# Optimization experiments

Measured on AMD Instinct MI355X. Metric: run time of the kernel, lower is better.

The kernel has to match this reference:

```python
import jax, jax.numpy as jnp
import numpy as np

B, C_IN, C_OUT, T, R, CO = 8, 64, 64, 32, 32, 32


def setup_inputs() -> dict:
    key = jax.random.key(0)
    ks = jax.random.split(key, 8)
    scale = 1.0 / np.sqrt(C_IN)  # nn.Linear default uniform(-1/sqrt(in), 1/sqrt(in))
    w = lambda k: jax.random.uniform(k, (C_OUT, C_IN), jnp.float32, -scale, scale)
    return {
        "x": jax.random.normal(ks[0], (B, C_IN, T, R, CO), jnp.float32),
        "w_self": w(ks[1]),
        "w_tp": w(ks[2]),
        "w_tm": w(ks[3]),
        "w_rp": w(ks[4]),
        "w_rm": w(ks[5]),
        "w_cp": w(ks[6]),
        "w_cm": w(ks[7]),
    }


def _proj(v, w):
    # v: [B, t, r, c, C_in], w: [C_out, C_in] (nn.Linear layout)
    return jnp.einsum('btrci,oi->btrco', v, w)


def _shift_pad(a, axis, front):
    # pad 1 slice at front (True) or back (False) along `axis` of a 5-D tensor
    pads = [(0, 0)] * 5
    pads[axis] = (1, 0) if front else (0, 1)
    return jnp.pad(a, pads)


def reference(x, w_self, w_tp, w_tm, w_rp, w_rm, w_cp, w_cm):
    xp = jnp.transpose(x, (0, 2, 3, 4, 1))  # [B, T, R, Co, C_in]
    out = _proj(xp, w_self)
    if xp.shape[1] > 1:
        out = out + _shift_pad(_proj(xp[:, :-1], w_tp), 1, True)
        out = out + _shift_pad(_proj(xp[:, 1:], w_tm), 1, False)
    if xp.shape[2] > 1:
        out = out + _shift_pad(_proj(xp[:, :, :-1], w_rp), 2, True)
        out = out + _shift_pad(_proj(xp[:, :, 1:], w_rm), 2, False)
    if xp.shape[3] > 1:
        out = out + _shift_pad(_proj(xp[:, :, :, :-1], w_cp), 3, True)
        out = out + _shift_pad(_proj(xp[:, :, :, 1:], w_cm), 3, False)
    return jnp.transpose(out, (0, 4, 1, 2, 3))  # [B, C_out, T, R, Co]
```

## Files before the change

kernel.cpp:

```cpp
#include <hip/hip_runtime.h>


#define SB 32768
#define CIN 64
#define COUT 64
#define NB 8

typedef short s16x8 __attribute__((ext_vector_type(8)));
typedef __bf16 bf16x8 __attribute__((ext_vector_type(8)));
typedef float f32x4 __attribute__((ext_vector_type(4)));

__device__ __forceinline__ unsigned f2bf(float f) {
    unsigned u = __float_as_uint(f);
    u += 0x7FFFu + ((u >> 16) & 1u);
    return u >> 16;
}
__device__ __forceinline__ unsigned pk2(float lo, float hi) {
    return f2bf(lo) | (f2bf(hi) << 16);
}

__global__ __launch_bounds__(256) void wprep_kernel(const float* __restrict__ w0,
                            const float* __restrict__ w1, const float* __restrict__ w2,
                            const float* __restrict__ w3, const float* __restrict__ w4,
                            const float* __restrict__ w5, const float* __restrict__ w6,
                            unsigned short* __restrict__ ws) {
    int tap = blockIdx.x;
    int tid = threadIdx.x;
    const float* w = (tap == 0) ? w0 : (tap == 1) ? w1 : (tap == 2) ? w2
                   : (tap == 3) ? w3 : (tap == 4) ? w4 : (tap == 5) ? w5 : w6;
    unsigned p[8];
#pragma unroll
    for (int j = 0; j < 8; ++j)
        p[j] = pk2(w[tid * 16 + 2 * j], w[tid * 16 + 2 * j + 1]);
    uint4* dp = (uint4*)(ws + tap * 4096 + tid * 16);
    dp[0] = make_uint4(p[0], p[1], p[2], p[3]);
    dp[1] = make_uint4(p[4], p[5], p[6], p[7]);
}

__global__ __launch_bounds__(256) void prep_kernel(const float* __restrict__ x,
                            const float* __restrict__ w0, const float* __restrict__ w1,
                            const float* __restrict__ w2, const float* __restrict__ w3,
                            const float* __restrict__ w4, const float* __restrict__ w5,
                            const float* __restrict__ w6,
                            unsigned short* __restrict__ ws) {
    int bid = blockIdx.x;
    int tid = threadIdx.x;
    if (bid >= 1024) {
        int tap = bid - 1024;
        const float* w = (tap == 0) ? w0 : (tap == 1) ? w1 : (tap == 2) ? w2
                       : (tap == 3) ? w3 : (tap == 4) ? w4 : (tap == 5) ? w5 : w6;
        unsigned p[8];
#pragma unroll
        for (int j = 0; j < 8; ++j)
            p[j] = pk2(w[tid * 16 + 2 * j], w[tid * 16 + 2 * j + 1]);
        uint4* dp = (uint4*)(ws + tap * 4096 + tid * 16);
        dp[0] = make_uint4(p[0], p[1], p[2], p[3]);
        dp[1] = make_uint4(p[4], p[5], p[6], p[7]);
        return;
    }
    __shared__ uint4 l[2048];
    int lbid = ((bid & 7) << 7) | (bid >> 3);
    int b = lbid >> 7;
    int sblk = (lbid & 127) << 8;
    unsigned short* xq = ws + 7 * 4096;
    const float* xp = x + (size_t)b * CIN * SB + sblk + tid;
#pragma unroll
    for (int c = 0; c < 4; ++c) {
        unsigned pk[8];
#pragma unroll
        for (int u = 0; u < 8; ++u)
            pk[u] = pk2(xp[(size_t)(c * 16 + 2 * u) * SB],
                        xp[(size_t)(c * 16 + 2 * u + 1) * SB]);
        l[tid * 8 + ((2 * c) ^ (tid & 7))] = make_uint4(pk[0], pk[1], pk[2], pk[3]);
        l[tid * 8 + ((2 * c + 1) ^ (tid & 7))] = make_uint4(pk[4], pk[5], pk[6], pk[7]);
    }
    __syncthreads();
    uint4* dst = (uint4*)(xq + ((size_t)b * SB + sblk) * 64);
#pragma unroll
    for (int k = 0; k < 8; ++k) {
        int idx = k * 256 + tid;
        int row = idx >> 3;
        int col = idx & 7;
        dst[idx] = l[row * 8 + (col ^ (row & 7))];
    }
}

__global__ __launch_bounds__(256) void conv2_kernel(const unsigned short* __restrict__ xq,
                                                    const unsigned short* __restrict__ wq,
                                                    float* __restrict__ out) {
    int bid = blockIdx.x;
    int lbid = ((bid & 7) << 7) | (bid >> 3);
    int b = lbid >> 7;
    int sblk = (lbid & 127) << 8;
    int tid = threadIdx.x;
    int lane = tid & 63;
    int wv = tid >> 6;
    int lo = lane & 15;
    int quad = lane >> 4;
    int sbase = sblk + wv * 64;
    int t = sblk >> 10;
    const unsigned short* xb = xq + (size_t)b * (CIN * SB);

    f32x4 acc[4][4];
#pragma unroll
    for (int mt = 0; mt < 4; ++mt)
#pragma unroll
        for (int nt = 0; nt < 4; ++nt)
            acc[mt][nt] = (f32x4){0.f, 0.f, 0.f, 0.f};

    int s_m[4], r_m[4], c_m[4];
#pragma unroll
    for (int mt = 0; mt < 4; ++mt) {
        int s = sbase + mt * 16 + lo;
        s_m[mt] = s;
        r_m[mt] = (s >> 5) & 31;
        c_m[mt] = s & 31;
    }

    auto load_b = [&](const unsigned short* wt, int ks, int nt) -> bf16x8 {
        const unsigned short* bp = wt + (nt * 16 + lo) * 64 + ks * 32 + quad * 8;
        return __builtin_bit_cast(bf16x8, *(const s16x8*)bp);
    };

    auto run_tap = [&](int tap, int d, const bool ok[4]) {
        const unsigned short* wt = wq + tap * 4096;
#pragma unroll
        for (int ks = 0; ks < 2; ++ks) {
            bf16x8 bf[4];
#pragma unroll
            for (int nt = 0; nt < 4; ++nt) bf[nt] = load_b(wt, ks, nt);
#pragma unroll
            for (int mt = 0; mt < 4; ++mt) {
                int s = s_m[mt] + d;
                s = s < 0 ? 0 : s;
                s = s > SB - 1 ? SB - 1 : s;
                s16x8 raw = *(const s16x8*)(xb + (size_t)s * 64 + ks * 32 + quad * 8);
                s16x8 zz = {0, 0, 0, 0, 0, 0, 0, 0};
                raw = ok[mt] ? raw : zz;
                bf16x8 af = __builtin_bit_cast(bf16x8, raw);
#pragma unroll
                for (int nt = 0; nt < 4; ++nt)
                    acc[mt][nt] = __builtin_amdgcn_mfma_f32_16x16x32_bf16(af, bf[nt], acc[mt][nt], 0, 0, 0);
            }
        }
    };

    {
        bool ok_all[4] = {true, true, true, true};
        run_tap(0, 0, ok_all);
        if (t > 0)  run_tap(1, -1024, ok_all);
        if (t < 31) run_tap(2, 1024, ok_all);
    }
    {
        bool ok[4];
#pragma unroll
        for (int mt = 0; mt < 4; ++mt) ok[mt] = (r_m[mt] > 0);
        run_tap(3, -32, ok);
#pragma unroll
        for (int mt = 0; mt < 4; ++mt) ok[mt] = (r_m[mt] < 31);
        run_tap(4, 32, ok);
#pragma unroll
        for (int mt = 0; mt < 4; ++mt) ok[mt] = (c_m[mt] > 0);
        run_tap(5, -1, ok);
#pragma unroll
        for (int mt = 0; mt < 4; ++mt) ok[mt] = (c_m[mt] < 31);
        run_tap(6, 1, ok);
    }

#pragma unroll
    for (int mt = 0; mt < 4; ++mt) {
#pragma unroll
        for (int nt = 0; nt < 4; ++nt) {
            int o = nt * 16 + lo;
            size_t off = ((size_t)(b * COUT + o)) * SB + sbase + mt * 16 + quad * 4;
            *(f32x4*)(out + off) = acc[mt][nt];
        }
    }
}

__global__ __launch_bounds__(256) void conv_kernel(const float* __restrict__ x,
                                                   const unsigned short* __restrict__ wq,
                                                   float* __restrict__ out) {
    __shared__ uint4 alds[2560];
    int bid = blockIdx.x;
    int b = bid >> 7;
    int sblk = (bid & 127) << 8;
    int tid = threadIdx.x;
    const float* xb = x + (size_t)b * CIN * SB;

    {
        int rl = 32 + tid;
        const float* xp = xb + sblk + tid;
#pragma unroll
        for (int c = 0; c < 4; ++c) {
            unsigned pk[8];
#pragma unroll
            for (int u = 0; u < 8; ++u)
                pk[u] = pk2(xp[(size_t)(c * 16 + 2 * u) * SB],
                            xp[(size_t)(c * 16 + 2 * u + 1) * SB]);
            alds[rl * 8 + ((2 * c) ^ (rl & 7))] = make_uint4(pk[0], pk[1], pk[2], pk[3]);
            alds[rl * 8 + ((2 * c + 1) ^ (rl & 7))] = make_uint4(pk[4], pk[5], pk[6], pk[7]);
        }
    }
    {
        int hrow = tid & 63;
        int rl = (hrow < 32) ? hrow : hrow + 256;
        int s = sblk - 32 + rl;
        s = max(0, min(SB - 1, s));
        int ic = tid >> 6;
        const float* xp = xb + s + (size_t)(ic * 16) * SB;
        unsigned pk[8];
#pragma unroll
        for (int u = 0; u < 8; ++u)
            pk[u] = pk2(xp[(size_t)(2 * u) * SB], xp[(size_t)(2 * u + 1) * SB]);
        alds[rl * 8 + ((2 * ic) ^ (rl & 7))] = make_uint4(pk[0], pk[1], pk[2], pk[3]);
        alds[rl * 8 + ((2 * ic + 1) ^ (rl & 7))] = make_uint4(pk[4], pk[5], pk[6], pk[7]);
    }
    __syncthreads();

    int lane = tid & 63;
    int wv = tid >> 6;
    int lo = lane & 15;
    int quad = lane >> 4;
    int sbase = sblk + wv * 64;
    int t = sblk >> 10;

    f32x4 acc[4][4];
#pragma unroll
    for (int mt = 0; mt < 4; ++mt)
#pragma unroll
        for (int nt = 0; nt < 4; ++nt)
            acc[mt][nt] = (f32x4){0.f, 0.f, 0.f, 0.f};

    int r_m[4], c_m[4], rl[4];
#pragma unroll
    for (int mt = 0; mt < 4; ++mt) {
        int s = sbase + mt * 16 + lo;
        r_m[mt] = (s >> 5) & 31;
        c_m[mt] = s & 31;
        rl[mt] = s - sblk + 32;
    }

    auto load_b = [&](const unsigned short* wt, int ks, int nt) -> bf16x8 {
        const unsigned short* bp = wt + (nt * 16 + lo) * 64 + ks * 32 + quad * 8;
        return __builtin_bit_cast(bf16x8, *(const s16x8*)bp);
    };

    auto run_tap_lds = [&](int tap, int d, const bool ok[4]) {
        const unsigned short* wt = wq + tap * 4096;
#pragma unroll
        for (int ks = 0; ks < 2; ++ks) {
            bf16x8 bf[4];
#pragma unroll
            for (int nt = 0; nt < 4; ++nt) bf[nt] = load_b(wt, ks, nt);
            int j = ks * 4 + quad;
#pragma unroll
            for (int mt = 0; mt < 4; ++mt) {
                int row = rl[mt] + d;
                s16x8 raw = *((const s16x8*)alds + row * 8 + (j ^ (row & 7)));
                s16x8 zz = {0, 0, 0, 0, 0, 0, 0, 0};
                raw = ok[mt] ? raw : zz;
                bf16x8 af = __builtin_bit_cast(bf16x8, raw);
#pragma unroll
                for (int nt = 0; nt < 4; ++nt)
                    acc[mt][nt] = __builtin_amdgcn_mfma_f32_16x16x32_bf16(af, bf[nt], acc[mt][nt], 0, 0, 0);
            }
        }
    };

    auto run_tap_gather = [&](int tap, int d) {
        const unsigned short* wt = wq + tap * 4096;
#pragma unroll
        for (int ks = 0; ks < 2; ++ks) {
            bf16x8 bf[4];
#pragma unroll
            for (int nt = 0; nt < 4; ++nt) bf[nt] = load_b(wt, ks, nt);
            const float* gp = xb + (size_t)(ks * 32 + quad * 8) * SB + d;
#pragma unroll
            for (int mt = 0; mt < 4; ++mt) {
                const float* ap = gp + sbase + mt * 16 + lo;
                unsigned pk[4];
#pragma unroll
                for (int u = 0; u < 4; ++u)
                    pk[u] = pk2(ap[(size_t)(2 * u) * SB], ap[(size_t)(2 * u + 1) * SB]);
                uint4 v = make_uint4(pk[0], pk[1], pk[2], pk[3]);
                bf16x8 af = __builtin_bit_cast(bf16x8, v);
#pragma unroll
                for (int nt = 0; nt < 4; ++nt)
                    acc[mt][nt] = __builtin_amdgcn_mfma_f32_16x16x32_bf16(af, bf[nt], acc[mt][nt], 0, 0, 0);
            }
        }
    };

    {
        bool ok_all[4] = {true, true, true, true};
        run_tap_lds(0, 0, ok_all);
    }
    if (t > 0)  run_tap_gather(1, -1024);
    if (t < 31) run_tap_gather(2, 1024);
    {
        bool ok[4];
#pragma unroll
        for (int mt = 0; mt < 4; ++mt) ok[mt] = (r_m[mt] > 0);
        run_tap_lds(3, -32, ok);
#pragma unroll
        for (int mt = 0; mt < 4; ++mt) ok[mt] = (r_m[mt] < 31);
        run_tap_lds(4, 32, ok);
#pragma unroll
        for (int mt = 0; mt < 4; ++mt) ok[mt] = (c_m[mt] > 0);
        run_tap_lds(5, -1, ok);
#pragma unroll
        for (int mt = 0; mt < 4; ++mt) ok[mt] = (c_m[mt] < 31);
        run_tap_lds(6, 1, ok);
    }

#pragma unroll
    for (int mt = 0; mt < 4; ++mt) {
#pragma unroll
        for (int nt = 0; nt < 4; ++nt) {
            int o = nt * 16 + lo;
            size_t off = ((size_t)(b * COUT + o)) * SB + sbase + mt * 16 + quad * 4;
            *(f32x4*)(out + off) = acc[mt][nt];
        }
    }
}

__global__ void fallback_kernel(const float* __restrict__ x,
                                const float* __restrict__ w0, const float* __restrict__ w1,
                                const float* __restrict__ w2, const float* __restrict__ w3,
                                const float* __restrict__ w4, const float* __restrict__ w5,
                                const float* __restrict__ w6,
                                float* __restrict__ out) {
    int bid = blockIdx.x;
    int b = bid >> 11;
    int og = (bid >> 7) & 15;
    int sblk = (bid & 127) << 8;
    int tid = threadIdx.x;
    __shared__ float wl[7][4][64];
    const float* wp[7] = {w0, w1, w2, w3, w4, w5, w6};
    for (int k = tid; k < 7 * 4 * 64; k += 256) {
        int tap = k >> 8, oo = (k >> 6) & 3, i = k & 63;
        wl[tap][oo][i] = wp[tap][(og * 4 + oo) * 64 + i];
    }
    __syncthreads();
    int s = sblk + tid;
    int t = s >> 10, r = (s >> 5) & 31, c = s & 31;
    const float* xb = x + (size_t)b * CIN * SB + s;
    float a0 = 0, a1 = 0, a2 = 0, a3 = 0;
    for (int i = 0; i < 64; ++i) {
        const float* xi = xb + (size_t)i * SB;
        float vs = xi[0];
        float vtp = (t > 0) ? xi[-1024] : 0.f;
        float vtm = (t < 31) ? xi[1024] : 0.f;
        float vrp = (r > 0) ? xi[-32] : 0.f;
        float vrm = (r < 31) ? xi[32] : 0.f;
        float vcp = (c > 0) ? xi[-1] : 0.f;
        float vcm = (c < 31) ? xi[1] : 0.f;
        a0 += wl[0][0][i] * vs + wl[1][0][i] * vtp + wl[2][0][i] * vtm + wl[3][0][i] * vrp + wl[4][0][i] * vrm + wl[5][0][i] * vcp + wl[6][0][i] * vcm;
        a1 += wl[0][1][i] * vs + wl[1][1][i] * vtp + wl[2][1][i] * vtm + wl[3][1][i] * vrp + wl[4][1][i] * vrm + wl[5][1][i] * vcp + wl[6][1][i] * vcm;
        a2 += wl[0][2][i] * vs + wl[1][2][i] * vtp + wl[2][2][i] * vtm + wl[3][2][i] * vrp + wl[4][2][i] * vrm + wl[5][2][i] * vcp + wl[6][2][i] * vcm;
        a3 += wl[0][3][i] * vs + wl[1][3][i] * vtp + wl[2][3][i] * vtm + wl[3][3][i] * vrp + wl[4][3][i] * vrm + wl[5][3][i] * vcp + wl[6][3][i] * vcm;
    }
    size_t obase = ((size_t)b * COUT + og * 4) * SB + s;
    out[obase] = a0;
    out[obase + SB] = a1;
    out[obase + 2 * (size_t)SB] = a2;
    out[obase + 3 * (size_t)SB] = a3;
}

extern "C" void kernel_launch(void* const* d_in, const int* in_sizes, int n_in,
                              void* d_out, int out_size, void* d_ws, size_t ws_size,
                              hipStream_t stream) {
    const float* x = (const float*)d_in[0];
    const float* w0 = (const float*)d_in[1];
    const float* w1 = (const float*)d_in[2];
    const float* w2 = (const float*)d_in[3];
    const float* w3 = (const float*)d_in[4];
    const float* w4 = (const float*)d_in[5];
    const float* w5 = (const float*)d_in[6];
    const float* w6 = (const float*)d_in[7];
    float* out = (float*)d_out;

    size_t need_w = (size_t)7 * 4096 * 2;
    size_t need_full = need_w + (size_t)NB * CIN * SB * 2;
    if (d_ws != nullptr && ws_size >= need_full) {
        unsigned short* wsp = (unsigned short*)d_ws;
        prep_kernel<<<1031, 256, 0, stream>>>(x, w0, w1, w2, w3, w4, w5, w6, wsp);
        conv2_kernel<<<1024, 256, 0, stream>>>(wsp + 7 * 4096, wsp, out);
    } else if (d_ws != nullptr && ws_size >= need_w) {
        unsigned short* wsp = (unsigned short*)d_ws;
        wprep_kernel<<<7, 256, 0, stream>>>(w0, w1, w2, w3, w4, w5, w6, wsp);
        conv_kernel<<<1024, 256, 0, stream>>>(x, wsp, out);
    } else {
        fallback_kernel<<<8 * 16 * 128, 256, 0, stream>>>(x, w0, w1, w2, w3, w4, w5, w6, out);
    }
}
```

Before: 178.9 us.

## Stage bf16 activation tile in LDS and split output channels across waves

The bf16 transpose prep kernel drops its LDS staging and uses more blocks, each thread reading float2 pairs and writing packed channel groups directly. The conv kernel now uses 512 threads: it loads a haloed 320-row activation tile into swizzled LDS for the self, r and c taps, and gathers only the t taps from global memory. Each wave computes half of the output channels and keeps all seven taps' weight fragments in registers. The aim is to cut redundant global reads of neighbour rows and per-tap weight reloads, at the cost of more registers and a block-wide barrier.

```diff
diff --git a/kernel.cpp b/kernel.cpp
--- a/kernel.cpp
+++ b/kernel.cpp
@@ -37,7 +37,7 @@
     dp[1] = make_uint4(p[4], p[5], p[6], p[7]);
 }
 
-__global__ __launch_bounds__(256) void prep_kernel(const float* __restrict__ x,
+__global__ __launch_bounds__(256) void prep2_kernel(const float* __restrict__ x,
                             const float* __restrict__ w0, const float* __restrict__ w1,
                             const float* __restrict__ w2, const float* __restrict__ w3,
                             const float* __restrict__ w4, const float* __restrict__ w5,
@@ -45,8 +45,8 @@
                             unsigned short* __restrict__ ws) {
     int bid = blockIdx.x;
     int tid = threadIdx.x;
-    if (bid >= 1024) {
-        int tap = bid - 1024;
+    if (bid >= 4096) {
+        int tap = bid - 4096;
         const float* w = (tap == 0) ? w0 : (tap == 1) ? w1 : (tap == 2) ? w2
                        : (tap == 3) ? w3 : (tap == 4) ? w4 : (tap == 5) ? w5 : w6;
         unsigned p[8];
@@ -58,36 +58,31 @@
         dp[1] = make_uint4(p[4], p[5], p[6], p[7]);
         return;
     }
-    __shared__ uint4 l[2048];
-    int lbid = ((bid & 7) << 7) | (bid >> 3);
-    int b = lbid >> 7;
-    int sblk = (lbid & 127) << 8;
+    int lbid = ((bid & 7) << 9) | (bid >> 3);
+    int b = lbid >> 9;
+    int i = (lbid & 511) * 256 + tid;
+    int cg = i & 7;
+    int s = (i >> 3) * 2;
+    const float* xb = x + (size_t)b * CIN * SB;
     unsigned short* xq = ws + 7 * 4096;
-    const float* xp = x + (size_t)b * CIN * SB + sblk + tid;
-#pragma unroll
-    for (int c = 0; c < 4; ++c) {
-        unsigned pk[8];
-#pragma unroll
-        for (int u = 0; u < 8; ++u)
-            pk[u] = pk2(xp[(size_t)(c * 16 + 2 * u) * SB],
-                        xp[(size_t)(c * 16 + 2 * u + 1) * SB]);
-        l[tid * 8 + ((2 * c) ^ (tid & 7))] = make_uint4(pk[0], pk[1], pk[2], pk[3]);
-        l[tid * 8 + ((2 * c + 1) ^ (tid & 7))] = make_uint4(pk[4], pk[5], pk[6], pk[7]);
-    }
-    __syncthreads();
-    uint4* dst = (uint4*)(xq + ((size_t)b * SB + sblk) * 64);
-#pragma unroll
-    for (int k = 0; k < 8; ++k) {
-        int idx = k * 256 + tid;
-        int row = idx >> 3;
-        int col = idx & 7;
-        dst[idx] = l[row * 8 + (col ^ (row & 7))];
-    }
-}
-
-__global__ __launch_bounds__(256) void conv2_kernel(const unsigned short* __restrict__ xq,
-                                                    const unsigned short* __restrict__ wq,
-                                                    float* __restrict__ out) {
+    unsigned pa[4], pb[4];
+#pragma unroll
+    for (int u = 0; u < 4; ++u) {
+        int ch = cg * 8 + 2 * u;
+        float2 v0 = *(const float2*)(xb + (size_t)ch * SB + s);
+        float2 v1 = *(const float2*)(xb + (size_t)(ch + 1) * SB + s);
+        pa[u] = pk2(v0.x, v1.x);
+        pb[u] = pk2(v0.y, v1.y);
+    }
+    uint4* dst = (uint4*)(xq + ((size_t)b * SB + s) * 64 + cg * 8);
+    dst[0] = make_uint4(pa[0], pa[1], pa[2], pa[3]);
+    dst[8] = make_uint4(pb[0], pb[1], pb[2], pb[3]);
+}
+
+__global__ __launch_bounds__(512, 8) void conv3_kernel(const unsigned short* __restrict__ xq,
+                                                       const unsigned short* __restrict__ wq,
+                                                       float* __restrict__ out) {
+    __shared__ uint4 alds[2560];
     int bid = blockIdx.x;
     int lbid = ((bid & 7) << 7) | (bid >> 3);
     int b = lbid >> 7;
@@ -97,81 +92,113 @@
     int wv = tid >> 6;
     int lo = lane & 15;
     int quad = lane >> 4;
-    int sbase = sblk + wv * 64;
+    int oh = wv & 1;
+    int sq = wv >> 1;
+    int sbase = sblk + sq * 64;
     int t = sblk >> 10;
     const unsigned short* xb = xq + (size_t)b * (CIN * SB);
 
-    f32x4 acc[4][4];
+    bf16x8 bq[7][2][2];
+#pragma unroll
+    for (int tap = 0; tap < 7; ++tap)
+#pragma unroll
+        for (int ks = 0; ks < 2; ++ks)
+#pragma unroll
+            for (int nt = 0; nt < 2; ++nt) {
+                const unsigned short* bp = wq + tap * 4096
+                    + (oh * 32 + nt * 16 + lo) * 64 + ks * 32 + quad * 8;
+                bq[tap][ks][nt] = __builtin_bit_cast(bf16x8, *(const s16x8*)bp);
+            }
+
+    {
+        const uint4* src = (const uint4*)xb;
+#pragma unroll
+        for (int u = 0; u < 5; ++u) {
+            int idx = u * 512 + tid;
+            int row = idx >> 3;
+            int col = idx & 7;
+            int gr = sblk - 32 + row;
+            gr = gr < 0 ? 0 : (gr > SB - 1 ? SB - 1 : gr);
+            uint4 v = src[gr * 8 + col];
+            alds[row * 8 + (col ^ (row & 7))] = v;
+        }
+    }
+    __syncthreads();
+
+    f32x4 acc[4][2];
 #pragma unroll
     for (int mt = 0; mt < 4; ++mt)
 #pragma unroll
-        for (int nt = 0; nt < 4; ++nt)
+        for (int nt = 0; nt < 2; ++nt)
             acc[mt][nt] = (f32x4){0.f, 0.f, 0.f, 0.f};
 
-    int s_m[4], r_m[4], c_m[4];
+    int s_m[4], r_m[4], c_m[4], rl[4];
 #pragma unroll
     for (int mt = 0; mt < 4; ++mt) {
         int s = sbase + mt * 16 + lo;
         s_m[mt] = s;
         r_m[mt] = (s >> 5) & 31;
         c_m[mt] = s & 31;
-    }
-
-    auto load_b = [&](const unsigned short* wt, int ks, int nt) -> bf16x8 {
-        const unsigned short* bp = wt + (nt * 16 + lo) * 64 + ks * 32 + quad * 8;
-        return __builtin_bit_cast(bf16x8, *(const s16x8*)bp);
-    };
-
-    auto run_tap = [&](int tap, int d, const bool ok[4]) {
-        const unsigned short* wt = wq + tap * 4096;
+        rl[mt] = s - sblk + 32;
+    }
+
+    const s16x8 zz = {0, 0, 0, 0, 0, 0, 0, 0};
+
+    auto run_tap_lds = [&](const bf16x8 (&bt)[2][2], int d, const bool (&ok)[4]) {
 #pragma unroll
         for (int ks = 0; ks < 2; ++ks) {
-            bf16x8 bf[4];
-#pragma unroll
-            for (int nt = 0; nt < 4; ++nt) bf[nt] = load_b(wt, ks, nt);
 #pragma unroll
             for (int mt = 0; mt < 4; ++mt) {
-                int s = s_m[mt] + d;
-                s = s < 0 ? 0 : s;
-                s = s > SB - 1 ? SB - 1 : s;
-                s16x8 raw = *(const s16x8*)(xb + (size_t)s * 64 + ks * 32 + quad * 8);
-                s16x8 zz = {0, 0, 0, 0, 0, 0, 0, 0};
+                int row = rl[mt] + d;
+                s16x8 raw = *((const s16x8*)alds + row * 8 + ((ks * 4 + quad) ^ (row & 7)));
                 raw = ok[mt] ? raw : zz;
                 bf16x8 af = __builtin_bit_cast(bf16x8, raw);
-#pragma unroll
-                for (int nt = 0; nt < 4; ++nt)
-                    acc[mt][nt] = __builtin_amdgcn_mfma_f32_16x16x32_bf16(af, bf[nt], acc[mt][nt], 0, 0, 0);
+                acc[mt][0] = __builtin_amdgcn_mfma_f32_16x16x32_bf16(af, bt[ks][0], acc[mt][0], 0, 0, 0);
+                acc[mt][1] = __builtin_amdgcn_mfma_f32_16x16x32_bf16(af, bt[ks][1], acc[mt][1], 0, 0, 0);
             }
         }
     };
 
+    auto run_tap_gather = [&](const bf16x8 (&bt)[2][2], int d) {
+#pragma unroll
+        for (int ks = 0; ks < 2; ++ks) {
+#pragma unroll
+            for (int mt = 0; mt < 4; ++mt) {
+                s16x8 raw = *(const s16x8*)(xb + (size_t)(s_m[mt] + d) * 64 + ks * 32 + quad * 8);
+                bf16x8 af = __builtin_bit_cast(bf16x8, raw);
+                acc[mt][0] = __builtin_amdgcn_mfma_f32_16x16x32_bf16(af, bt[ks][0], acc[mt][0], 0, 0, 0);
+                acc[mt][1] = __builtin_amdgcn_mfma_f32_16x16x32_bf16(af, bt[ks][1], acc[mt][1], 0, 0, 0);
+            }
+        }
+    };
+
     {
         bool ok_all[4] = {true, true, true, true};
-        run_tap(0, 0, ok_all);
-        if (t > 0)  run_tap(1, -1024, ok_all);
-        if (t < 31) run_tap(2, 1024, ok_all);
-    }
+        run_tap_lds(bq[0], 0, ok_all);
+    }
+    if (t > 0)  run_tap_gather(bq[1], -1024);
+    if (t < 31) run_tap_gather(bq[2], 1024);
     {
         bool ok[4];
 #pragma unroll
         for (int mt = 0; mt < 4; ++mt) ok[mt] = (r_m[mt] > 0);
-        run_tap(3, -32, ok);
+        run_tap_lds(bq[3], -32, ok);
 #pragma unroll
         for (int mt = 0; mt < 4; ++mt) ok[mt] = (r_m[mt] < 31);
-        run_tap(4, 32, ok);
+        run_tap_lds(bq[4], 32, ok);
 #pragma unroll
         for (int mt = 0; mt < 4; ++mt) ok[mt] = (c_m[mt] > 0);
-        run_tap(5, -1, ok);
+        run_tap_lds(bq[5], -1, ok);
 #pragma unroll
         for (int mt = 0; mt < 4; ++mt) ok[mt] = (c_m[mt] < 31);
-        run_tap(6, 1, ok);
+        run_tap_lds(bq[6], 1, ok);
     }
 
 #pragma unroll
     for (int mt = 0; mt < 4; ++mt) {
 #pragma unroll
-        for (int nt = 0; nt < 4; ++nt) {
-            int o = nt * 16 + lo;
+        for (int nt = 0; nt < 2; ++nt) {
+            int o = oh * 32 + nt * 16 + lo;
             size_t off = ((size_t)(b * COUT + o)) * SB + sbase + mt * 16 + quad * 4;
             *(f32x4*)(out + off) = acc[mt][nt];
         }
@@ -258,8 +285,8 @@
             for (int mt = 0; mt < 4; ++mt) {
                 int row = rl[mt] + d;
                 s16x8 raw = *((const s16x8*)alds + row * 8 + (j ^ (row & 7)));
-                s16x8 zz = {0, 0, 0, 0, 0, 0, 0, 0};
-                raw = ok[mt] ? raw : zz;
+                s16x8 zx = {0, 0, 0, 0, 0, 0, 0, 0};
+                raw = ok[mt] ? raw : zx;
                 bf16x8 af = __builtin_bit_cast(bf16x8, raw);
 #pragma unroll
                 for (int nt = 0; nt < 4; ++nt)
@@ -385,8 +412,8 @@
     size_t need_full = need_w + (size_t)NB * CIN * SB * 2;
     if (d_ws != nullptr && ws_size >= need_full) {
         unsigned short* wsp = (unsigned short*)d_ws;
-        prep_kernel<<<1031, 256, 0, stream>>>(x, w0, w1, w2, w3, w4, w5, w6, wsp);
-        conv2_kernel<<<1024, 256, 0, stream>>>(wsp + 7 * 4096, wsp, out);
+        prep2_kernel<<<4103, 256, 0, stream>>>(x, w0, w1, w2, w3, w4, w5, w6, wsp);
+        conv3_kernel<<<1024, 512, 0, stream>>>(wsp + 7 * 4096, wsp, out);
     } else if (d_ws != nullptr && ws_size >= need_w) {
         unsigned short* wsp = (unsigned short*)d_ws;
         wprep_kernel<<<7, 256, 0, stream>>>(w0, w1, w2, w3, w4, w5, w6, wsp);
```

Result: slower. 302.0 us (+68.8%).

## Rewrite x transpose-prep without LDS and halve conv tile per block

Applied to the files above, without the earlier changes.

The prep kernel now converts x to bf16 channel-last with no shared-memory staging. Each thread reads float2 pairs from eight channels and writes two 16-byte chunks, and the grid grows to 4096 blocks. The conv kernel processes 32 spatial positions per wave instead of 64, doubling the block count to 2048 and preloading both k-slices of the weights per tap. This aims for more parallelism and occupancy and less LDS and sync overhead, at the cost of less weight reuse per block and more scattered prep stores.

```diff
diff --git a/kernel.cpp b/kernel.cpp
--- a/kernel.cpp
+++ b/kernel.cpp
@@ -37,7 +37,7 @@
     dp[1] = make_uint4(p[4], p[5], p[6], p[7]);
 }
 
-__global__ __launch_bounds__(256) void prep_kernel(const float* __restrict__ x,
+__global__ __launch_bounds__(256) void prep2_kernel(const float* __restrict__ x,
                             const float* __restrict__ w0, const float* __restrict__ w1,
                             const float* __restrict__ w2, const float* __restrict__ w3,
                             const float* __restrict__ w4, const float* __restrict__ w5,
@@ -45,8 +45,8 @@
                             unsigned short* __restrict__ ws) {
     int bid = blockIdx.x;
     int tid = threadIdx.x;
-    if (bid >= 1024) {
-        int tap = bid - 1024;
+    if (bid >= 4096) {
+        int tap = bid - 4096;
         const float* w = (tap == 0) ? w0 : (tap == 1) ? w1 : (tap == 2) ? w2
                        : (tap == 3) ? w3 : (tap == 4) ? w4 : (tap == 5) ? w5 : w6;
         unsigned p[8];
@@ -58,117 +58,112 @@
         dp[1] = make_uint4(p[4], p[5], p[6], p[7]);
         return;
     }
-    __shared__ uint4 l[2048];
-    int lbid = ((bid & 7) << 7) | (bid >> 3);
-    int b = lbid >> 7;
-    int sblk = (lbid & 127) << 8;
+    int lbid = ((bid & 7) << 9) | (bid >> 3);
+    int b = lbid >> 9;
+    int i = (lbid & 511) * 256 + tid;
+    int cg = i & 7;
+    int s = (i >> 3) * 2;
+    const float* xb = x + (size_t)b * CIN * SB;
     unsigned short* xq = ws + 7 * 4096;
-    const float* xp = x + (size_t)b * CIN * SB + sblk + tid;
-#pragma unroll
-    for (int c = 0; c < 4; ++c) {
-        unsigned pk[8];
-#pragma unroll
-        for (int u = 0; u < 8; ++u)
-            pk[u] = pk2(xp[(size_t)(c * 16 + 2 * u) * SB],
-                        xp[(size_t)(c * 16 + 2 * u + 1) * SB]);
-        l[tid * 8 + ((2 * c) ^ (tid & 7))] = make_uint4(pk[0], pk[1], pk[2], pk[3]);
-        l[tid * 8 + ((2 * c + 1) ^ (tid & 7))] = make_uint4(pk[4], pk[5], pk[6], pk[7]);
-    }
-    __syncthreads();
-    uint4* dst = (uint4*)(xq + ((size_t)b * SB + sblk) * 64);
-#pragma unroll
-    for (int k = 0; k < 8; ++k) {
-        int idx = k * 256 + tid;
-        int row = idx >> 3;
-        int col = idx & 7;
-        dst[idx] = l[row * 8 + (col ^ (row & 7))];
-    }
-}
-
-__global__ __launch_bounds__(256) void conv2_kernel(const unsigned short* __restrict__ xq,
+    unsigned pa[4], pb[4];
+#pragma unroll
+    for (int u = 0; u < 4; ++u) {
+        int ch = cg * 8 + 2 * u;
+        float2 v0 = *(const float2*)(xb + (size_t)ch * SB + s);
+        float2 v1 = *(const float2*)(xb + (size_t)(ch + 1) * SB + s);
+        pa[u] = pk2(v0.x, v1.x);
+        pb[u] = pk2(v0.y, v1.y);
+    }
+    uint4* dst = (uint4*)(xq + ((size_t)b * SB + s) * 64 + cg * 8);
+    dst[0] = make_uint4(pa[0], pa[1], pa[2], pa[3]);
+    dst[8] = make_uint4(pb[0], pb[1], pb[2], pb[3]);
+}
+
+__global__ __launch_bounds__(256) void conv4_kernel(const unsigned short* __restrict__ xq,
                                                     const unsigned short* __restrict__ wq,
                                                     float* __restrict__ out) {
     int bid = blockIdx.x;
-    int lbid = ((bid & 7) << 7) | (bid >> 3);
-    int b = lbid >> 7;
-    int sblk = (lbid & 127) << 8;
+    int lbid = ((bid & 7) << 8) | (bid >> 3);
+    int b = lbid >> 8;
+    int sblk = (lbid & 255) << 7;
     int tid = threadIdx.x;
     int lane = tid & 63;
     int wv = tid >> 6;
     int lo = lane & 15;
     int quad = lane >> 4;
-    int sbase = sblk + wv * 64;
+    int sbase = sblk + wv * 32;
     int t = sblk >> 10;
     const unsigned short* xb = xq + (size_t)b * (CIN * SB);
 
-    f32x4 acc[4][4];
-#pragma unroll
-    for (int mt = 0; mt < 4; ++mt)
+    f32x4 acc[2][4];
+#pragma unroll
+    for (int mt = 0; mt < 2; ++mt)
 #pragma unroll
         for (int nt = 0; nt < 4; ++nt)
             acc[mt][nt] = (f32x4){0.f, 0.f, 0.f, 0.f};
 
-    int s_m[4], r_m[4], c_m[4];
-#pragma unroll
-    for (int mt = 0; mt < 4; ++mt) {
+    int s_m[2], r_m[2], c_m[2];
+#pragma unroll
+    for (int mt = 0; mt < 2; ++mt) {
         int s = sbase + mt * 16 + lo;
         s_m[mt] = s;
         r_m[mt] = (s >> 5) & 31;
         c_m[mt] = s & 31;
     }
 
-    auto load_b = [&](const unsigned short* wt, int ks, int nt) -> bf16x8 {
-        const unsigned short* bp = wt + (nt * 16 + lo) * 64 + ks * 32 + quad * 8;
-        return __builtin_bit_cast(bf16x8, *(const s16x8*)bp);
-    };
-
-    auto run_tap = [&](int tap, int d, const bool ok[4]) {
+    const s16x8 zz = {0, 0, 0, 0, 0, 0, 0, 0};
+
+    auto run_tap = [&](int tap, int d, const bool (&ok)[2]) {
         const unsigned short* wt = wq + tap * 4096;
+        bf16x8 bf[2][4];
+#pragma unroll
+        for (int ks = 0; ks < 2; ++ks)
+#pragma unroll
+            for (int nt = 0; nt < 4; ++nt) {
+                const unsigned short* bp = wt + (nt * 16 + lo) * 64 + ks * 32 + quad * 8;
+                bf[ks][nt] = __builtin_bit_cast(bf16x8, *(const s16x8*)bp);
+            }
 #pragma unroll
         for (int ks = 0; ks < 2; ++ks) {
-            bf16x8 bf[4];
-#pragma unroll
-            for (int nt = 0; nt < 4; ++nt) bf[nt] = load_b(wt, ks, nt);
-#pragma unroll
-            for (int mt = 0; mt < 4; ++mt) {
+#pragma unroll
+            for (int mt = 0; mt < 2; ++mt) {
                 int s = s_m[mt] + d;
                 s = s < 0 ? 0 : s;
                 s = s > SB - 1 ? SB - 1 : s;
                 s16x8 raw = *(const s16x8*)(xb + (size_t)s * 64 + ks * 32 + quad * 8);
-                s16x8 zz = {0, 0, 0, 0, 0, 0, 0, 0};
                 raw = ok[mt] ? raw : zz;
                 bf16x8 af = __builtin_bit_cast(bf16x8, raw);
 #pragma unroll
                 for (int nt = 0; nt < 4; ++nt)
-                    acc[mt][nt] = __builtin_amdgcn_mfma_f32_16x16x32_bf16(af, bf[nt], acc[mt][nt], 0, 0, 0);
+                    acc[mt][nt] = __builtin_amdgcn_mfma_f32_16x16x32_bf16(af, bf[ks][nt], acc[mt][nt], 0, 0, 0);
             }
         }
     };
 
     {
-        bool ok_all[4] = {true, true, true, true};
+        bool ok_all[2] = {true, true};
         run_tap(0, 0, ok_all);
         if (t > 0)  run_tap(1, -1024, ok_all);
         if (t < 31) run_tap(2, 1024, ok_all);
     }
     {
-        bool ok[4];
-#pragma unroll
-        for (int mt = 0; mt < 4; ++mt) ok[mt] = (r_m[mt] > 0);
+        bool ok[2];
+#pragma unroll
+        for (int mt = 0; mt < 2; ++mt) ok[mt] = (r_m[mt] > 0);
         run_tap(3, -32, ok);
 #pragma unroll
-        for (int mt = 0; mt < 4; ++mt) ok[mt] = (r_m[mt] < 31);
+        for (int mt = 0; mt < 2; ++mt) ok[mt] = (r_m[mt] < 31);
         run_tap(4, 32, ok);
 #pragma unroll
-        for (int mt = 0; mt < 4; ++mt) ok[mt] = (c_m[mt] > 0);
+        for (int mt = 0; mt < 2; ++mt) ok[mt] = (c_m[mt] > 0);
         run_tap(5, -1, ok);
 #pragma unroll
-        for (int mt = 0; mt < 4; ++mt) ok[mt] = (c_m[mt] < 31);
+        for (int mt = 0; mt < 2; ++mt) ok[mt] = (c_m[mt] < 31);
         run_tap(6, 1, ok);
     }
 
 #pragma unroll
-    for (int mt = 0; mt < 4; ++mt) {
+    for (int mt = 0; mt < 2; ++mt) {
 #pragma unroll
         for (int nt = 0; nt < 4; ++nt) {
             int o = nt * 16 + lo;
@@ -258,8 +253,8 @@
             for (int mt = 0; mt < 4; ++mt) {
                 int row = rl[mt] + d;
                 s16x8 raw = *((const s16x8*)alds + row * 8 + (j ^ (row & 7)));
-                s16x8 zz = {0, 0, 0, 0, 0, 0, 0, 0};
-                raw = ok[mt] ? raw : zz;
+                s16x8 zx = {0, 0, 0, 0, 0, 0, 0, 0};
+                raw = ok[mt] ? raw : zx;
                 bf16x8 af = __builtin_bit_cast(bf16x8, raw);
 #pragma unroll
                 for (int nt = 0; nt < 4; ++nt)
@@ -385,8 +380,8 @@
     size_t need_full = need_w + (size_t)NB * CIN * SB * 2;
     if (d_ws != nullptr && ws_size >= need_full) {
         unsigned short* wsp = (unsigned short*)d_ws;
-        prep_kernel<<<1031, 256, 0, stream>>>(x, w0, w1, w2, w3, w4, w5, w6, wsp);
-        conv2_kernel<<<1024, 256, 0, stream>>>(wsp + 7 * 4096, wsp, out);
+        prep2_kernel<<<4103, 256, 0, stream>>>(x, w0, w1, w2, w3, w4, w5, w6, wsp);
+        conv4_kernel<<<2048, 256, 0, stream>>>(wsp + 7 * 4096, wsp, out);
     } else if (d_ws != nullptr && ws_size >= need_w) {
         unsigned short* wsp = (unsigned short*)d_ws;
         wprep_kernel<<<7, 256, 0, stream>>>(w0, w1, w2, w3, w4, w5, w6, wsp);
```

Result: slower. 208.2 us (+16.3%).
